# Kernel optimization log

Hardware: AMD Instinct MI355X
Metric: run time of the kernel (lower is better)

The kernel has to match this reference:

```python
import jax, jax.numpy as jnp
import numpy as np

B, R, C, S, K = 8, 16, 512, 512, 64
GAMMA = 0.99
DPP = 1 * (8192 // 512)  # n_device * n_block_per_update = 16


def setup_inputs() -> dict:
    key = jax.random.key(0)
    k1, k2, k3 = jax.random.split(key, 3)
    vecs = jax.random.normal(k1, (B, R, C, K), dtype=jnp.float32)
    c_sum = jax.random.normal(k2, (S, K), dtype=jnp.float32)
    # realistic EMA usage counts, strictly positive
    c_count = jax.random.uniform(k3, (S,), dtype=jnp.float32) * 100.0 + 1.0
    return {"vecs": vecs, "c_sum": c_sum, "c_count": c_count}


def reference(vecs, c_sum, c_count):
    sg = jax.lax.stop_gradient
    st = lambda x: x - sg(x)

    # codebook from EMA stats (stop-gradient, as in _get_codebook)
    c = sg(c_sum / jnp.clip(c_count[:, None], 0.01))  # [S,K]

    # get_shortcodes: squared distances via three contractions (no cdist materialized beyond [B,R,C,S])
    diffs2 = (jnp.sum(jnp.square(vecs), axis=-1)[..., None]
              - 2.0 * jnp.einsum('brck,sk->brcs', vecs, c)
              + jnp.sum(jnp.square(c), axis=-1)[None, None, None, :])  # [B,R,C,S]
    z = jnp.argmin(diffs2, axis=-1).astype(jnp.int32)  # [B,R,C]
    errs2 = jax.nn.relu(jnp.min(diffs2, axis=-1))      # [B,R,C]

    # get_codewords: gather codewords (equivalent to take_along_axis in original)
    cz = jnp.take(c, z, axis=0)  # [B,R,C,K]

    # straight-through estimator
    vecs_hat = sg(cz) + st(vecs)

    # commitment loss (head_type == 'shga': no extra sum over axis 1)
    l_commit = jnp.mean(errs2)

    # codebook EMA-target loss; targets only ever appear under stop_gradient
    vflat = sg(vecs).reshape(-1, K)
    zflat = z.reshape(-1)
    c_sum_hat = DPP * jax.ops.segment_sum(vflat, zflat, num_segments=S)          # [S,K]
    c_count_hat = DPP * jax.ops.segment_sum(jnp.ones_like(zflat, jnp.float32), zflat, num_segments=S)  # [S]
    c_sum_tgt = (1.0 - GAMMA) * c_sum_hat + GAMMA * sg(c_sum)
    c_count_tgt = (1.0 - GAMMA) * c_count_hat + GAMMA * sg(c_count)
    l_codebook = (jnp.sum(sg(c_sum - c_sum_tgt) * st(c_sum))
                  + jnp.sum(sg(c_count - c_count_tgt) * st(c_count)))

    return (vecs_hat, z, l_commit, l_codebook, errs2)
```

## Files before the change

### kernel.cpp

```cpp
#include <hip/hip_runtime.h>

#define NVEC   65536
#define KDIM   64
#define SDIM   512

#define Z_OFF       4194304
#define LCOMMIT_OFF 4259840
#define LCODE_OFF   4259841
#define E_OFF       4259842

typedef _Float16 half8   __attribute__((ext_vector_type(8)));
typedef float    floatx16 __attribute__((ext_vector_type(16)));


__global__ void vq_prep(const float* __restrict__ c_sum,
                        const float* __restrict__ c_count,
                        float* __restrict__ c32,
                        float* __restrict__ cnorm,
                        _Float16* __restrict__ cbf16,
                        float* __restrict__ out) {
    int s = blockIdx.x;
    int k = threadIdx.x;
    float cnt = c_count[s];
    float inv = 1.0f / fmaxf(cnt, 0.01f);
    float x = c_sum[s * KDIM + k] * inv;
    c32[s * KDIM + k] = x;
    float sq = x * x;
    #pragma unroll
    for (int off = 32; off > 0; off >>= 1)
        sq += __shfl_down(sq, off);
    if (k == 0) cnorm[s] = sq;

    __shared__ _Float16 hb[64], lb[64];
    _Float16 hi = (_Float16)x;
    float hiF = (float)hi;
    _Float16 lo = (_Float16)(x - hiF);
    hb[k] = hi; lb[k] = lo;
    __syncthreads();
    if (k < 16) {
        int p  = k >> 3;
        int qh = k & 7;
        int k0 = (qh >> 1) * 16 + (qh & 1) * 8;
        const _Float16* srcb = (p ? lb : hb) + k0;
        half8 v;
        #pragma unroll
        for (int j = 0; j < 8; ++j) v[j] = srcb[j];
        size_t chunk = ((size_t)(s >> 5) * 16 + p * 8 + qh) * 32 + (s & 31);
        *(half8*)(cbf16 + chunk * 8) = v;
    }
    if (s == 0 && k == 0) {
        out[LCOMMIT_OFF] = 0.0f;
        out[LCODE_OFF]   = 0.0f;
    }
}

__global__ __launch_bounds__(128, 2) void vq_main(const float* __restrict__ vecs,
                                                  const _Float16* __restrict__ cbf16,
                                                  const float* __restrict__ c32,
                                                  const float* __restrict__ cnorm,
                                                  float* __restrict__ out) {
    __shared__ __align__(16) _Float16 cw[16384];
    __shared__ float cnL[128];
    __shared__ float vnL[2][32];
    __shared__ int   zL[2][32];

    const int tx   = threadIdx.x;
    const int lane = tx & 63;
    const int w    = tx >> 6;
    const int col  = lane & 31;
    const int h    = lane >> 5;
    const int wvec = (int)blockIdx.x * 64 + w * 32;

    half8 ahi[4], alo[4];
    float vnp = 0.0f;
    const float* arow = vecs + (size_t)(wvec + col) * KDIM + h * 8;
    #pragma unroll
    for (int q = 0; q < 4; ++q) {
        float4 x0 = *(const float4*)(arow + q * 16);
        float4 x1 = *(const float4*)(arow + q * 16 + 4);
        #define CVT(X, J) { float xx = (X); _Float16 hi5 = (_Float16)xx; \
                            float hf = (float)hi5; ahi[q][J] = hi5; \
                            alo[q][J] = (_Float16)(xx - hf); vnp += xx * xx; }
        CVT(x0.x, 0) CVT(x0.y, 1) CVT(x0.z, 2) CVT(x0.w, 3)
        CVT(x1.x, 4) CVT(x1.y, 5) CVT(x1.z, 6) CVT(x1.w, 7)
        #undef CVT
    }
    vnp += __shfl_xor(vnp, 32);
    if (h == 0) vnL[w][col] = vnp;

    float bq[16];
    int   bi[16];
    #pragma unroll
    for (int r = 0; r < 16; ++r) { bq[r] = 3.4e38f; bi[r] = 0; }

    for (int t = 0; t < 4; ++t) {
        __syncthreads();
        const float4* src = (const float4*)(cbf16 + (size_t)t * 16384);
        float4* dst = (float4*)cw;
        #pragma unroll 4
        for (int i = 0; i < 16; ++i)
            dst[i * 128 + tx] = src[i * 128 + tx];
        if (tx < 128) cnL[tx] = cnorm[t * 128 + tx];
        __syncthreads();

        #pragma unroll
        for (int sub = 0; sub < 4; ++sub) {
            const _Float16* bb = cw + sub * 4096 + lane * 8;
            floatx16 a0 = {0.0f}, a1 = {0.0f}, a2 = {0.0f};
            #pragma unroll
            for (int q = 0; q < 4; ++q) {
                half8 bh = *(const half8*)(bb + q * 512);
                half8 bl = *(const half8*)(bb + 2048 + q * 512);
                a0 = __builtin_amdgcn_mfma_f32_32x32x16_f16(ahi[q], bh, a0, 0, 0, 0);
                a1 = __builtin_amdgcn_mfma_f32_32x32x16_f16(alo[q], bh, a1, 0, 0, 0);
                a2 = __builtin_amdgcn_mfma_f32_32x32x16_f16(ahi[q], bl, a2, 0, 0, 0);
            }
            float cnv = cnL[sub * 32 + col];
            int   n   = t * 128 + sub * 32 + col;
            #pragma unroll
            for (int r = 0; r < 16; ++r) {
                float dot = (a0[r] + a1[r]) + a2[r];
                float qd  = fmaf(-2.0f, dot, cnv);
                if (qd < bq[r]) { bq[r] = qd; bi[r] = n; }
            }
        }
    }

    #pragma unroll
    for (int r = 0; r < 16; ++r) {
        float v = bq[r]; int i = bi[r];
        #pragma unroll
        for (int off = 16; off > 0; off >>= 1) {
            float ov = __shfl_xor(v, off);
            int   oi = __shfl_xor(i, off);
            if (ov < v || (ov == v && oi < i)) { v = ov; i = oi; }
        }
        bq[r] = v; bi[r] = i;
    }

    if (col == 0) {
        float esum = 0.0f;
        #pragma unroll
        for (int r = 0; r < 16; ++r) {
            int row = (r & 3) + 8 * (r >> 2) + 4 * h;
            int vid = wvec + row;
            float err = fmaxf(vnL[w][row] + bq[r], 0.0f);
            out[Z_OFF + vid] = (float)bi[r];
            out[E_OFF + vid] = err;
            zL[w][row] = bi[r];
            esum += err;
        }
        atomicAdd(out + LCOMMIT_OFF, esum * (1.0f / (float)NVEC));
    }

    #pragma unroll
    for (int it = 0; it < 8; ++it) {
        int row = it * 4 + (lane >> 4);
        int c4  = lane & 15;
        int z   = zL[w][row];
        float4 val = *(const float4*)(c32 + (size_t)z * KDIM + c4 * 4);
        *(float4*)(out + (size_t)(wvec + row) * KDIM + c4 * 4) = val;
    }
}

extern "C" void kernel_launch(void* const* d_in, const int* in_sizes, int n_in,
                              void* d_out, int out_size, void* d_ws, size_t ws_size,
                              hipStream_t stream) {
    const float* vecs    = (const float*)d_in[0];
    const float* c_sum   = (const float*)d_in[1];
    const float* c_count = (const float*)d_in[2];
    float* out = (float*)d_out;

    float*    c32   = (float*)d_ws;
    float*    cnorm = c32 + SDIM * KDIM;
    _Float16* cbf16 = (_Float16*)(cnorm + SDIM);

    vq_prep<<<SDIM, KDIM, 0, stream>>>(c_sum, c_count, c32, cnorm, cbf16, out);
    vq_main<<<NVEC / 64, 128, 0, stream>>>(vecs, cbf16, c32, cnorm, out);
}
```

Baseline: 120.0 us.

## Double-buffer codebook tiles via async LDS DMA and fold norm into MFMA accumulator

Codebook tiles now go into shared memory with direct global-to-LDS loads (global_load_lds) into two ping-pong buffers, so the next tile's load overlaps MFMA work on the current one. This removes the register round-trip and one barrier per tile. The block grows to 256 threads (4 waves, 128 vectors) and all codebook norms are preloaded once. The -0.5*||c||² term now seeds the accumulator, the two correction MFMAs share one accumulator, and the argmin becomes an argmax, which trims per-element VALU work. The cost is twice the LDS per block, which may lower occupancy, and the correctness relies on the barrier waiting for the async LDS loads.

Result: faster. 116.1 us (-3.3%).

```diff
diff --git a/kernel.cpp b/kernel.cpp
--- a/kernel.cpp
+++ b/kernel.cpp
@@ -1,15 +1,15 @@
 #include <hip/hip_runtime.h>
 
-#define NVEC   65536
-#define KDIM   64
-#define SDIM   512
+#define NVEC 65536
+#define KDIM 64
+#define SDIM 512
 
 #define Z_OFF       4194304
 #define LCOMMIT_OFF 4259840
 #define LCODE_OFF   4259841
 #define E_OFF       4259842
 
-typedef _Float16 half8   __attribute__((ext_vector_type(8)));
+typedef _Float16 half8    __attribute__((ext_vector_type(8)));
 typedef float    floatx16 __attribute__((ext_vector_type(16)));
 
 
@@ -54,22 +54,36 @@
     }
 }
 
-__global__ __launch_bounds__(128, 2) void vq_main(const float* __restrict__ vecs,
+__global__ __launch_bounds__(256, 2) void vq_main(const float* __restrict__ vecs,
                                                   const _Float16* __restrict__ cbf16,
                                                   const float* __restrict__ c32,
                                                   const float* __restrict__ cnorm,
                                                   float* __restrict__ out) {
-    __shared__ __align__(16) _Float16 cw[16384];
-    __shared__ float cnL[128];
-    __shared__ float vnL[2][32];
-    __shared__ int   zL[2][32];
+    __shared__ __align__(16) _Float16 cw[2][16384];
+    __shared__ float cnL[512];
+    __shared__ float vnL[4][32];
+    __shared__ int   zL[4][32];
 
     const int tx   = threadIdx.x;
     const int lane = tx & 63;
     const int w    = tx >> 6;
     const int col  = lane & 31;
     const int h    = lane >> 5;
-    const int wvec = (int)blockIdx.x * 64 + w * 32;
+    const int wvec = (int)blockIdx.x * 128 + w * 32;
+
+    #define DMA_TILE(buf, t)                                                      \
+    {                                                                             \
+        const _Float16* _src = cbf16 + (size_t)(t) * 16384 + w * 4096 + lane * 8; \
+        _Float16* _dst = &cw[buf][w * 4096 + lane * 8];                           \
+        _Pragma("unroll")                                                         \
+        for (int _i = 0; _i < 8; ++_i)                                            \
+            __builtin_amdgcn_global_load_lds(                                     \
+                (const __attribute__((address_space(1))) void*)(_src + _i * 512), \
+                (__attribute__((address_space(3))) void*)(_dst + _i * 512),       \
+                16, 0, 0);                                                        \
+    }
+
+    DMA_TILE(0, 0)
 
     half8 ahi[4], alo[4];
     float vnp = 0.0f;
@@ -88,54 +102,53 @@
     vnp += __shfl_xor(vnp, 32);
     if (h == 0) vnL[w][col] = vnp;
 
-    float bq[16];
+    cnL[tx]       = cnorm[tx];
+    cnL[tx + 256] = cnorm[tx + 256];
+
+    float bm[16];
     int   bi[16];
     #pragma unroll
-    for (int r = 0; r < 16; ++r) { bq[r] = 3.4e38f; bi[r] = 0; }
+    for (int r = 0; r < 16; ++r) { bm[r] = -3.4e38f; bi[r] = 0; }
 
     for (int t = 0; t < 4; ++t) {
         __syncthreads();
-        const float4* src = (const float4*)(cbf16 + (size_t)t * 16384);
-        float4* dst = (float4*)cw;
-        #pragma unroll 4
-        for (int i = 0; i < 16; ++i)
-            dst[i * 128 + tx] = src[i * 128 + tx];
-        if (tx < 128) cnL[tx] = cnorm[t * 128 + tx];
-        __syncthreads();
+        if (t < 3) DMA_TILE((t + 1) & 1, t + 1)
 
+        const _Float16* cwb = cw[t & 1];
         #pragma unroll
         for (int sub = 0; sub < 4; ++sub) {
-            const _Float16* bb = cw + sub * 4096 + lane * 8;
-            floatx16 a0 = {0.0f}, a1 = {0.0f}, a2 = {0.0f};
+            const _Float16* bb = cwb + sub * 4096 + lane * 8;
+            float ci = -0.5f * cnL[t * 128 + sub * 32 + col];
+            floatx16 a0, a1;
+            #pragma unroll
+            for (int r = 0; r < 16; ++r) { a0[r] = ci; a1[r] = 0.0f; }
             #pragma unroll
             for (int q = 0; q < 4; ++q) {
                 half8 bh = *(const half8*)(bb + q * 512);
                 half8 bl = *(const half8*)(bb + 2048 + q * 512);
                 a0 = __builtin_amdgcn_mfma_f32_32x32x16_f16(ahi[q], bh, a0, 0, 0, 0);
                 a1 = __builtin_amdgcn_mfma_f32_32x32x16_f16(alo[q], bh, a1, 0, 0, 0);
-                a2 = __builtin_amdgcn_mfma_f32_32x32x16_f16(ahi[q], bl, a2, 0, 0, 0);
+                a1 = __builtin_amdgcn_mfma_f32_32x32x16_f16(ahi[q], bl, a1, 0, 0, 0);
             }
-            float cnv = cnL[sub * 32 + col];
-            int   n   = t * 128 + sub * 32 + col;
+            int n = t * 128 + sub * 32 + col;
             #pragma unroll
             for (int r = 0; r < 16; ++r) {
-                float dot = (a0[r] + a1[r]) + a2[r];
-                float qd  = fmaf(-2.0f, dot, cnv);
-                if (qd < bq[r]) { bq[r] = qd; bi[r] = n; }
+                float m = a0[r] + a1[r];
+                if (m > bm[r]) { bm[r] = m; bi[r] = n; }
             }
         }
     }
 
     #pragma unroll
     for (int r = 0; r < 16; ++r) {
-        float v = bq[r]; int i = bi[r];
+        float v = bm[r]; int i = bi[r];
         #pragma unroll
         for (int off = 16; off > 0; off >>= 1) {
             float ov = __shfl_xor(v, off);
             int   oi = __shfl_xor(i, off);
-            if (ov < v || (ov == v && oi < i)) { v = ov; i = oi; }
+            if (ov > v || (ov == v && oi < i)) { v = ov; i = oi; }
         }
-        bq[r] = v; bi[r] = i;
+        bm[r] = v; bi[r] = i;
     }
 
     if (col == 0) {
@@ -144,7 +157,7 @@
         for (int r = 0; r < 16; ++r) {
             int row = (r & 3) + 8 * (r >> 2) + 4 * h;
             int vid = wvec + row;
-            float err = fmaxf(vnL[w][row] + bq[r], 0.0f);
+            float err = fmaxf(vnL[w][row] - 2.0f * bm[r], 0.0f);
             out[Z_OFF + vid] = (float)bi[r];
             out[E_OFF + vid] = err;
             zL[w][row] = bi[r];
@@ -161,6 +174,7 @@
         float4 val = *(const float4*)(c32 + (size_t)z * KDIM + c4 * 4);
         *(float4*)(out + (size_t)(wvec + row) * KDIM + c4 * 4) = val;
     }
+    #undef DMA_TILE
 }
 
 extern "C" void kernel_launch(void* const* d_in, const int* in_sizes, int n_in,
@@ -176,5 +190,5 @@
     _Float16* cbf16 = (_Float16*)(cnorm + SDIM);
 
     vq_prep<<<SDIM, KDIM, 0, stream>>>(c_sum, c_count, c32, cnorm, cbf16, out);
-    vq_main<<<NVEC / 64, 128, 0, stream>>>(vecs, cbf16, c32, cnorm, out);
+    vq_main<<<NVEC / 128, 256, 0, stream>>>(vecs, cbf16, c32, cnorm, out);
 }
```
